# Performance work log

Hardware: AMD Instinct MI355X
Metric: run time of the kernel (lower is better)

The kernel has to match this reference:

```python
import jax, jax.numpy as jnp
import numpy as np

N, E, B, D = 8192, 32768, 64, 64   # nodes, edges, graphs, hidden dim
FN, FE, EH = 32, 16, 128           # node feat, edge feat, edge-MLP hidden
STEPS, S2S = 4, 5                  # message passes, set2set steps
EPS = 1e-5


def bn(x, g, b):
    # BatchNorm1d forward with batch statistics (training-mode math, biased var)
    m = x.mean(0)
    v = x.var(0)
    return (x - m) * jax.lax.rsqrt(v + EPS) * g + b


def setup_inputs() -> dict:
    key = jax.random.key(0)
    ks = iter(jax.random.split(key, 48))
    def nrm(shape, s=0.1):
        return jax.random.normal(next(ks), shape, jnp.float32) * s
    return {
        "x": jax.random.normal(next(ks), (N, FN), jnp.float32),
        "edge_attr": jax.random.normal(next(ks), (E, FE), jnp.float32),
        "edge_index": jax.random.randint(next(ks), (2, E), 0, N),
        "batch": jnp.sort(jax.random.randint(next(ks), (N,), 0, B)),
        "lin0_W": nrm((FN, D)), "lin0_b": nrm((D,)),
        "bn0_g": jnp.ones(D), "bn0_b": jnp.zeros(D),
        "e1_W": nrm((FE, EH)), "e1_b": nrm((EH,)),
        "ebn_g": jnp.ones(EH), "ebn_b": jnp.zeros(EH),
        "e2_W": nrm((EH, D * D), 0.02), "e2_b": nrm((D * D,), 0.02),
        "root_W": nrm((D, D)), "root_b": nrm((D,)),
        "gru_Wih": nrm((D, 3 * D)), "gru_Whh": nrm((D, 3 * D)),
        "gru_bih": nrm((3 * D,)), "gru_bhh": nrm((3 * D,)),
        "lstm_Wih": nrm((2 * D, 4 * D)), "lstm_Whh": nrm((D, 4 * D)),
        "lstm_bih": nrm((4 * D,)), "lstm_bhh": nrm((4 * D,)),
        "f1_W": nrm((2 * D, 256)), "f1_b": nrm((256,)), "f1_g": jnp.ones(256), "f1_bt": jnp.zeros(256),
        "f2_W": nrm((256, 128)), "f2_b": nrm((128,)), "f2_g": jnp.ones(128), "f2_bt": jnp.zeros(128),
        "f3_W": nrm((128, 32)), "f3_b": nrm((32,)), "f3_g": jnp.ones(32), "f3_bt": jnp.zeros(32),
        "fo_W": nrm((32, 1)), "fo_b": nrm((1,)),
    }


def _forward(x, edge_attr, edge_index, batch,
             lin0_W, lin0_b, bn0_g, bn0_b,
             e1_W, e1_b, ebn_g, ebn_b, e2_W, e2_b,
             root_W, root_b,
             gru_Wih, gru_Whh, gru_bih, gru_bhh,
             lstm_Wih, lstm_Whh, lstm_bih, lstm_bhh,
             f1_W, f1_b, f1_g, f1_bt,
             f2_W, f2_b, f2_g, f2_bt,
             f3_W, f3_b, f3_g, f3_bt,
             fo_W, fo_b):
    src, dst = edge_index[0], edge_index[1]

    x0 = jax.nn.relu(bn(x @ lin0_W + lin0_b, bn0_g, bn0_b))  # [N, D]

    # Edge NN: per-edge weight matrix [E, D, D] (edge_attr is constant across passes)
    eh = jax.nn.relu(bn(edge_attr @ e1_W + e1_b, ebn_g, ebn_b))
    We = (eh @ e2_W + e2_b).reshape(E, D, D)

    cnt = jnp.clip(jax.ops.segment_sum(jnp.ones((E,), x.dtype), dst, num_segments=N), 1.0)

    h = x0
    xo = x0
    for _ in range(STEPS):
        # NNConv (aggr='mean', root weight + bias) then ReLU
        msg = jnp.einsum('ei,eio->eo', xo[src], We)                     # [E, D]
        agg = jax.ops.segment_sum(msg, dst, num_segments=N) / cnt[:, None]
        m = jax.nn.relu(agg + xo @ root_W + root_b)
        # GRU cell (seq len 1): gates r, z, n
        gi = m @ gru_Wih + gru_bih
        gh = h @ gru_Whh + gru_bhh
        ir, iz, inn = jnp.split(gi, 3, -1)
        hr, hz, hn = jnp.split(gh, 3, -1)
        r = jax.nn.sigmoid(ir + hr)
        z = jax.nn.sigmoid(iz + hz)
        n = jnp.tanh(inn + r * hn)
        h = (1.0 - z) * n + z * h
        xo = h  # dropout is identity in eval mode

    # Set2Set pooling: LSTM + segment-softmax attention over ragged graphs
    qs = jnp.zeros((B, 2 * D), x.dtype)
    hl = jnp.zeros((B, D), x.dtype)
    cl = jnp.zeros((B, D), x.dtype)
    for _ in range(S2S):
        g = qs @ lstm_Wih + lstm_bih + hl @ lstm_Whh + lstm_bhh
        i_, f_, g_, o_ = jnp.split(g, 4, -1)
        cl = jax.nn.sigmoid(f_) * cl + jax.nn.sigmoid(i_) * jnp.tanh(g_)
        hl = jax.nn.sigmoid(o_) * jnp.tanh(cl)
        q = hl                                                           # [B, D]
        e = jnp.sum(xo * q[batch], -1)                                   # [N]
        emax = jax.lax.stop_gradient(jax.ops.segment_max(e, batch, num_segments=B))
        a = jnp.exp(e - emax[batch])
        a = a / (jax.ops.segment_sum(a, batch, num_segments=B)[batch] + 1e-16)
        rsum = jax.ops.segment_sum(a[:, None] * xo, batch, num_segments=B)
        qs = jnp.concatenate([q, rsum], -1)                              # [B, 2D]

    # FCNN head: Linear+BN+ReLU x3, then Linear -> 1
    y = jax.nn.relu(bn(qs @ f1_W + f1_b, f1_g, f1_bt))
    y = jax.nn.relu(bn(y @ f2_W + f2_b, f2_g, f2_bt))
    y = jax.nn.relu(bn(y @ f3_W + f3_b, f3_g, f3_bt))
    return (y @ fo_W + fo_b).reshape(-1)                                 # [B]


def reference(x, edge_attr, edge_index, batch,
              lin0_W, lin0_b, bn0_g, bn0_b,
              e1_W, e1_b, ebn_g, ebn_b, e2_W, e2_b,
              root_W, root_b,
              gru_Wih, gru_Whh, gru_bih, gru_bhh,
              lstm_Wih, lstm_Whh, lstm_bih, lstm_bhh,
              f1_W, f1_b, f1_g, f1_bt,
              f2_W, f2_b, f2_g, f2_bt,
              f3_W, f3_b, f3_g, f3_bt,
              fo_W, fo_b):
    return _forward(x, edge_attr, edge_index, batch,
                    lin0_W, lin0_b, bn0_g, bn0_b,
                    e1_W, e1_b, ebn_g, ebn_b, e2_W, e2_b,
                    root_W, root_b,
                    gru_Wih, gru_Whh, gru_bih, gru_bhh,
                    lstm_Wih, lstm_Whh, lstm_bih, lstm_bhh,
                    f1_W, f1_b, f1_g, f1_bt,
                    f2_W, f2_b, f2_g, f2_bt,
                    f3_W, f3_b, f3_g, f3_bt,
                    fo_W, fo_b)
```

## Files before the change

### kernel.cpp

```cpp
#include <hip/hip_runtime.h>
#include <hip/hip_bf16.h>


#define N_  8192
#define E_  32768
#define B_  64
#define D_  64
#define FN_ 32
#define FE_ 16
#define EH_ 128

typedef _Float16 half8 __attribute__((ext_vector_type(8)));
typedef float    f32x4 __attribute__((ext_vector_type(4)));

__device__ __forceinline__ float sigmf(float x) { return 1.f / (1.f + expf(-x)); }

#if __has_builtin(__builtin_amdgcn_global_load_lds)
#define HAVE_GLDS 1
__device__ __forceinline__ void gl2lds16(const void* g, void* l) {
  __builtin_amdgcn_global_load_lds(
      (const __attribute__((address_space(1))) void*)g,
      (__attribute__((address_space(3))) void*)l, 16, 0, 0);
}
#else
#define HAVE_GLDS 0
#endif


__global__ __launch_bounds__(256) void k_pre1(const float* __restrict__ x,
    const float* __restrict__ lin0W, const float* __restrict__ lin0b,
    const float* __restrict__ ea, const float* __restrict__ e1W, const float* __restrict__ e1b,
    const int* __restrict__ dstI, const int* __restrict__ batch,
    float* __restrict__ t0, float* __restrict__ t1,
    int* __restrict__ cnt_i, int* __restrict__ nodecnt) {
  const int bid = blockIdx.x, t = threadIdx.x;
  if (bid < 2048) {
    int gid = bid * 256 + t;
    int n = gid >> 6, d = gid & 63;
    const float* xr = x + (size_t)n * FN_;
    float a = lin0b[d];
    #pragma unroll
    for (int i = 0; i < FN_; ++i) a += xr[i] * lin0W[i * 64 + d];
    t0[gid] = a;
  } else if (bid < 18432) {
    int gid = (bid - 2048) * 256 + t;
    int n = gid >> 7, j = gid & 127;
    const float* er = ea + (size_t)n * FE_;
    float a = e1b[j];
    #pragma unroll
    for (int i = 0; i < FE_; ++i) a += er[i] * e1W[i * 128 + j];
    t1[gid] = a;
  } else if (bid < 18560) {
    atomicAdd(&cnt_i[dstI[(bid - 18432) * 256 + t]], 1);
  } else {
    atomicAdd(&nodecnt[batch[(bid - 18560) * 256 + t]], 1);
  }
}


__global__ __launch_bounds__(256) void k_stats(const float* __restrict__ t0,
    const float* __restrict__ t1, float* __restrict__ mean0, float* __restrict__ rstd0,
    float* __restrict__ meanE, float* __restrict__ rstdE) {
  const int bid = blockIdx.x;
  const float* in; int rows, cols, d; float* mo; float* ro;
  if (bid < 64) { in = t0; rows = N_; cols = 64; d = bid; mo = mean0; ro = rstd0; }
  else { in = t1; rows = E_; cols = 128; d = bid - 64; mo = meanE; ro = rstdE; }
  float s = 0.f, s2 = 0.f;
  for (int n = threadIdx.x; n < rows; n += 256) {
    float v = in[(size_t)n * cols + d];
    s += v; s2 += v * v;
  }
  #pragma unroll
  for (int off = 32; off; off >>= 1) { s += __shfl_xor(s, off); s2 += __shfl_xor(s2, off); }
  __shared__ float ls[4], ls2[4];
  int w = threadIdx.x >> 6;
  if ((threadIdx.x & 63) == 0) { ls[w] = s; ls2[w] = s2; }
  __syncthreads();
  if (threadIdx.x == 0) {
    float S = ls[0] + ls[1] + ls[2] + ls[3], S2 = ls2[0] + ls2[1] + ls2[2] + ls2[3];
    float mu = S / rows;
    float va = S2 / rows - mu * mu;
    mo[d] = mu;
    ro[d] = rsqrtf(va + 1e-5f);
  }
}


__global__ __launch_bounds__(256) void k_pre3(const float* __restrict__ t0,
    const float* __restrict__ mean0, const float* __restrict__ rstd0,
    const float* __restrict__ bn0g, const float* __restrict__ bn0b,
    float* __restrict__ x0, float* __restrict__ hb,
    const float* __restrict__ t1, const float* __restrict__ meanE,
    const float* __restrict__ rstdE, const float* __restrict__ ebng,
    const float* __restrict__ ebnb, _Float16* __restrict__ ehq,
    const float* __restrict__ e2W, half8* __restrict__ w2p8,
    const float* __restrict__ gWih, const float* __restrict__ gWhh,
    half8* __restrict__ pWih, half8* __restrict__ pWhh,
    const float* __restrict__ e2b, const float* __restrict__ rootW,
    half8* __restrict__ pE2R) {
  const int bid = blockIdx.x, t = threadIdx.x;
  if (bid < 2048) {
    int gid = bid * 256 + t;
    int d = gid & 63;
    float v = fmaxf(0.f, (t0[gid] - mean0[d]) * rstd0[d] * bn0g[d] + bn0b[d]);
    x0[gid] = v; hb[gid] = v;
  } else if (bid < 18432) {
    int gid = (bid - 2048) * 256 + t;
    int d = gid & 127;
    float v = fmaxf(0.f, (t1[gid] - meanE[d]) * rstdE[d] * ebng[d] + ebnb[d]);
    ehq[gid] = (_Float16)v;
  } else if (bid < 18688) {
    int tt = (bid - 18432) * 256 + t;
    int l = tt & 63, nf = (tt >> 6) & 3, kf = (tt >> 8) & 3, i = tt >> 10;
    half8 v;
    #pragma unroll
    for (int j = 0; j < 8; ++j) {
      int k = kf * 32 + ((l >> 4) << 3) + j;
      v[j] = (_Float16)e2W[(size_t)k * 4096 + i * 64 + (nf << 4) + (l & 15)];
    }
    w2p8[tt] = v;
  } else if (bid < 18700) {
    int tt2 = (bid - 18688) * 256 + t;
    int tab = (tt2 >= 1536);
    int rr = tab ? tt2 - 1536 : tt2;
    int lane = rr & 63, q = rr >> 6;
    int tile = q % 12, kf = q / 12;
    const float* W = tab ? gWhh : gWih;
    int col = tile * 16 + (lane & 15);
    half8 v;
    #pragma unroll
    for (int j = 0; j < 8; ++j) {
      int k = kf * 32 + ((lane >> 4) << 3) + j;
      v[j] = (_Float16)W[k * 192 + col];
    }
    (tab ? pWhh : pWih)[rr] = v;
  } else {
    int rr = (bid - 18700) * 256 + t;
    int lane = rr & 63, q = rr >> 6;
    int tile = q % 8, kf = q / 8;
    int col = tile * 16 + (lane & 15);
    half8 v;
    #pragma unroll
    for (int j = 0; j < 8; ++j) {
      int k = kf * 32 + ((lane >> 4) << 3) + j;
      v[j] = (_Float16)((col < 64) ? e2b[k * 64 + col] : rootW[k * 64 + (col - 64)]);
    }
    pE2R[rr] = v;
  }
}


__global__ __launch_bounds__(1024) void k_scans(const int* __restrict__ cnt,
    const int* __restrict__ nodecnt, int* __restrict__ row_start,
    int* __restrict__ cursor, float* __restrict__ cntf, int* __restrict__ gs) {
  __shared__ int sp[1024];
  int t = threadIdx.x;
  if (t == 0) {
    int a = 0;
    for (int b = 0; b < B_; ++b) { gs[b] = a; a += nodecnt[b]; }
    gs[B_] = a;
  }
  int v[8]; int s = 0;
  #pragma unroll
  for (int j = 0; j < 8; ++j) { v[j] = cnt[t * 8 + j]; s += v[j]; }
  sp[t] = s;
  __syncthreads();
  for (int off = 1; off < 1024; off <<= 1) {
    int a = (t >= off) ? sp[t - off] : 0;
    __syncthreads();
    sp[t] += a;
    __syncthreads();
  }
  int run = sp[t] - s;
  #pragma unroll
  for (int j = 0; j < 8; ++j) {
    row_start[t * 8 + j] = run;
    cursor[t * 8 + j] = run;
    cntf[t * 8 + j] = fmaxf(1.0f, (float)v[j]);
    run += v[j];
  }
  if (t == 1023) row_start[N_] = run;
}

__global__ __launch_bounds__(256) void k_fillnl(const int* __restrict__ dstI,
    int* __restrict__ cursor, int* __restrict__ csr,
    const float* __restrict__ x0, const float* __restrict__ e2b,
    const float* __restrict__ rootW, const float* __restrict__ rootb,
    float* __restrict__ P2, float* __restrict__ R) {
  const int bid = blockIdx.x, t = threadIdx.x;
  if (bid < 128) {
    int e = bid * 256 + t;
    int pos = atomicAdd(&cursor[dstI[e]], 1);
    csr[pos] = e;
  } else {
    int gid = (bid - 128) * 256 + t;
    int n = gid >> 6, d = gid & 63;
    const float* xr = x0 + (size_t)n * 64;
    float ap = 0.f, ar = rootb[d];
    #pragma unroll 8
    for (int i = 0; i < 64; ++i) {
      float xv = xr[i];
      ap += xv * e2b[i * 64 + d];
      ar += xv * rootW[i * 64 + d];
    }
    P2[gid] = ap; R[gid] = ar;
  }
}


__global__ __launch_bounds__(256) void k_msg(const _Float16* __restrict__ ehq,
    const half8* __restrict__ w2p8, const float* __restrict__ xo, const float* __restrict__ P2,
    const int* __restrict__ srcI, float* __restrict__ msg) {
  __shared__ half8 bbuf[2][1024];
  __shared__ float xs[64][65];
  __shared__ int ssrc[64];
  const int tid = threadIdx.x;
  const int lane = tid & 63;
  const int w = tid >> 6;
  const int be = blockIdx.x * 64;

  if (tid < 64) ssrc[tid] = srcI[be + tid];
#if HAVE_GLDS
  #pragma unroll
  for (int c = 0; c < 4; ++c) gl2lds16(w2p8 + c * 256 + tid, &bbuf[0][c * 256 + tid]);
#endif
  __syncthreads();
  for (int r = w; r < 64; r += 4) xs[r][lane] = xo[(size_t)ssrc[r] * 64 + lane];

  half8 A[4][4];
  #pragma unroll
  for (int rt = 0; rt < 4; ++rt) {
    const _Float16* ap = ehq + (size_t)(be + rt * 16 + (lane & 15)) * 128 + ((lane >> 4) << 3);
    #pragma unroll
    for (int kf = 0; kf < 4; ++kf) A[rt][kf] = *(const half8*)(ap + kf * 32);
  }
#if !HAVE_GLDS
  #pragma unroll
  for (int c = 0; c < 4; ++c) bbuf[0][c * 256 + tid] = w2p8[c * 256 + tid];
#endif

  f32x4 acc[4] = {{0.f,0.f,0.f,0.f},{0.f,0.f,0.f,0.f},{0.f,0.f,0.f,0.f},{0.f,0.f,0.f,0.f}};
  __syncthreads();

  for (int i = 0; i < 64; ++i) {
    const int inext = (i < 63) ? i + 1 : 63;
    const half8* gp = w2p8 + (size_t)inext * 1024;
#if HAVE_GLDS
    half8* nb = &bbuf[(i + 1) & 1][0];
    #pragma unroll
    for (int c = 0; c < 4; ++c) gl2lds16(gp + c * 256 + tid, nb + c * 256 + tid);
#else
    half8 p[4];
    #pragma unroll
    for (int c = 0; c < 4; ++c) p[c] = gp[c * 256 + tid];
#endif

    const half8* bb = bbuf[i & 1];
    half8 Bf[4];
    #pragma unroll
    for (int kf = 0; kf < 4; ++kf) Bf[kf] = bb[(kf * 4 + w) * 64 + lane];

    #pragma unroll
    for (int rt = 0; rt < 4; ++rt) {
      f32x4 C = {0.f, 0.f, 0.f, 0.f};
      #pragma unroll
      for (int kf = 0; kf < 4; ++kf)
        C = __builtin_amdgcn_mfma_f32_16x16x32_f16(A[rt][kf], Bf[kf], C, 0, 0, 0);
      const int rbase = rt * 16 + ((lane >> 4) << 2);
      #pragma unroll
      for (int r = 0; r < 4; ++r) acc[rt][r] += xs[rbase + r][i] * C[r];
    }
#if !HAVE_GLDS
    half8* nb = &bbuf[(i + 1) & 1][0];
    #pragma unroll
    for (int c = 0; c < 4; ++c) nb[c * 256 + tid] = p[c];
#endif
    __syncthreads();
  }

  const int col = (w << 4) + (lane & 15);
  #pragma unroll
  for (int rt = 0; rt < 4; ++rt) {
    const int rbase = rt * 16 + ((lane >> 4) << 2);
    #pragma unroll
    for (int r = 0; r < 4; ++r) {
      const int row = rbase + r;
      const int e = be + row;
      const int sn = ssrc[row];
      msg[(size_t)e * 64 + col] = acc[rt][r] + P2[(size_t)sn * 64 + col];
    }
  }
}


__global__ __launch_bounds__(256) void k_node(const float* __restrict__ msg,
    const int* __restrict__ csr, const int* __restrict__ row_start,
    const float* __restrict__ cntf,
    const half8* __restrict__ pWih, const half8* __restrict__ pWhh,
    const float* __restrict__ bih, const float* __restrict__ bhh,
    const half8* __restrict__ pE2R, const float* __restrict__ rootb,
    float* __restrict__ h, float* __restrict__ P2, float* __restrict__ R, int doPR) {
  __shared__ _Float16 sm16[16 * 72];
  __shared__ _Float16 sh16[16 * 72];
  __shared__ float sh32[16 * 64];
  __shared__ float sgi[16 * 208];
  __shared__ float sgh[16 * 208];
  const int t = threadIdx.x, lane = t & 63, w = t >> 6;
  const int n0 = blockIdx.x * 16;

  #pragma unroll
  for (int g = 0; g < 4; ++g) {
    int nl = g * 4 + w, n = n0 + nl;
    int e0 = row_start[n], e1 = row_start[n + 1];
    float acc = 0.f;
    for (int idx = e0; idx < e1; ++idx) acc += msg[(size_t)csr[idx] * 64 + lane];
    float mval = fmaxf(0.f, acc / cntf[n] + R[(size_t)n * 64 + lane]);
    float hval = h[(size_t)n * 64 + lane];
    sm16[nl * 72 + lane] = (_Float16)mval;
    sh16[nl * 72 + lane] = (_Float16)hval;
    sh32[nl * 64 + lane] = hval;
  }
  __syncthreads();

  {
    const _Float16* As = (w < 2) ? sm16 : sh16;
    const half8* pW = (w < 2) ? pWih : pWhh;
    float* sg_ = (w < 2) ? sgi : sgh;
    const int abase = (lane & 15) * 72 + ((lane >> 4) << 3);
    half8 A0 = *(const half8*)(As + abase);
    half8 A1 = *(const half8*)(As + abase + 32);
    const int tbase = (w & 1) * 6;
    #pragma unroll
    for (int tt = 0; tt < 6; ++tt) {
      int tile = tbase + tt;
      half8 B0 = pW[tile * 64 + lane];
      half8 B1 = pW[(12 + tile) * 64 + lane];
      f32x4 C = {0.f, 0.f, 0.f, 0.f};
      C = __builtin_amdgcn_mfma_f32_16x16x32_f16(A0, B0, C, 0, 0, 0);
      C = __builtin_amdgcn_mfma_f32_16x16x32_f16(A1, B1, C, 0, 0, 0);
      int col = tile * 16 + (lane & 15);
      int rb = (lane >> 4) << 2;
      #pragma unroll
      for (int r = 0; r < 4; ++r) sg_[(rb + r) * 208 + col] = C[r];
    }
  }
  __syncthreads();

  #pragma unroll
  for (int rep = 0; rep < 4; ++rep) {
    int idx = rep * 256 + t, j = idx >> 6, d = idx & 63;
    float rr = sigmf(sgi[j * 208 + d] + bih[d] + sgh[j * 208 + d] + bhh[d]);
    float zz = sigmf(sgi[j * 208 + 64 + d] + bih[64 + d] + sgh[j * 208 + 64 + d] + bhh[64 + d]);
    float nn = tanhf(sgi[j * 208 + 128 + d] + bih[128 + d]
                     + rr * (sgh[j * 208 + 128 + d] + bhh[128 + d]));
    float hv = (1.f - zz) * nn + zz * sh32[j * 64 + d];
    h[(size_t)(n0 + j) * 64 + d] = hv;
    sh16[j * 72 + d] = (_Float16)hv;
  }
  __syncthreads();

  if (doPR) {
    const int abase = (lane & 15) * 72 + ((lane >> 4) << 3);
    half8 A0 = *(const half8*)(sh16 + abase);
    half8 A1 = *(const half8*)(sh16 + abase + 32);
    #pragma unroll
    for (int tt = 0; tt < 2; ++tt) {
      int tile = w * 2 + tt;
      half8 B0 = pE2R[tile * 64 + lane];
      half8 B1 = pE2R[(8 + tile) * 64 + lane];
      f32x4 C = {0.f, 0.f, 0.f, 0.f};
      C = __builtin_amdgcn_mfma_f32_16x16x32_f16(A0, B0, C, 0, 0, 0);
      C = __builtin_amdgcn_mfma_f32_16x16x32_f16(A1, B1, C, 0, 0, 0);
      int c0 = tile * 16 + (lane & 15);
      int rb = (lane >> 4) << 2;
      #pragma unroll
      for (int r = 0; r < 4; ++r) {
        int n = n0 + rb + r;
        if (c0 < 64) P2[(size_t)n * 64 + c0] = C[r];
        else R[(size_t)n * 64 + (c0 - 64)] = C[r] + rootb[c0 - 64];
      }
    }
  }
}


#define SCAP 224

__global__ __launch_bounds__(256) void k_s2s(const float* __restrict__ xo,
    const int* __restrict__ gs,
    const float* __restrict__ Wih, const float* __restrict__ Whh,
    const float* __restrict__ bih, const float* __restrict__ bhh,
    float* __restrict__ qs_g) {
  __shared__ float sxo[SCAP * 65];
  __shared__ float sqs[128], shl[64], scl[64], sg[256];
  __shared__ float se[512];
  __shared__ float redm[4], ash[4], rsh[4][64];
  const int t = threadIdx.x;
  const int lane = t & 63, w = t >> 6;
  const int b = blockIdx.x;
  const int s0 = gs[b], cnt = gs[b + 1] - s0;
  const int cc = (cnt < SCAP) ? cnt : SCAP;

  for (int i = w; i < cc; i += 4) sxo[i * 65 + lane] = xo[(size_t)(s0 + i) * 64 + lane];
  if (t < 128) sqs[t] = 0.f;
  if (t < 64) { shl[t] = 0.f; scl[t] = 0.f; }
  __syncthreads();

  for (int it = 0; it < 5; ++it) {
    float a = bih[t] + bhh[t];
    #pragma unroll 8
    for (int k = 0; k < 128; ++k) a += sqs[k] * Wih[k * 256 + t];
    #pragma unroll 8
    for (int k = 0; k < 64; ++k)  a += shl[k] * Whh[k * 256 + t];
    sg[t] = a;
    __syncthreads();
    if (t < 64) {
      float i_ = sg[t], f_ = sg[64 + t], g_ = sg[128 + t], o_ = sg[192 + t];
      float cl = sigmf(f_) * scl[t] + sigmf(i_) * tanhf(g_);
      scl[t] = cl;
      shl[t] = sigmf(o_) * tanhf(cl);
    }
    __syncthreads();
    for (int i = t; i < cnt; i += 256) {
      float acc = 0.f;
      if (i < SCAP) {
        #pragma unroll 8
        for (int d = 0; d < 64; ++d) acc += sxo[i * 65 + d] * shl[d];
      } else {
        const float* xr = xo + (size_t)(s0 + i) * 64;
        #pragma unroll 8
        for (int d = 0; d < 64; ++d) acc += xr[d] * shl[d];
      }
      se[i] = acc;
    }
    __syncthreads();
    float mx = -INFINITY;
    for (int i = t; i < cnt; i += 256) mx = fmaxf(mx, se[i]);
    #pragma unroll
    for (int off = 32; off; off >>= 1) mx = fmaxf(mx, __shfl_xor(mx, off));
    if (lane == 0) redm[w] = mx;
    __syncthreads();
    const float gmax = fmaxf(fmaxf(redm[0], redm[1]), fmaxf(redm[2], redm[3]));
    float s = 0.f;
    for (int i = t; i < cnt; i += 256) {
      float aa = expf(se[i] - gmax);
      se[i] = aa;
      s += aa;
    }
    #pragma unroll
    for (int off = 32; off; off >>= 1) s += __shfl_xor(s, off);
    if (lane == 0) ash[w] = s;
    __syncthreads();
    const float gsum = ash[0] + ash[1] + ash[2] + ash[3];
    float racc = 0.f;
    for (int i = w; i < cnt; i += 4) {
      float aa = se[i];
      racc += (i < SCAP) ? aa * sxo[i * 65 + lane]
                         : aa * xo[(size_t)(s0 + i) * 64 + lane];
    }
    rsh[w][lane] = racc;
    __syncthreads();
    if (t < 64) {
      float rt_ = rsh[0][t] + rsh[1][t] + rsh[2][t] + rsh[3][t];
      sqs[t] = shl[t];
      sqs[64 + t] = rt_ / (gsum + 1e-16f);
    }
    __syncthreads();
  }
  if (t < 128) qs_g[b * 128 + t] = sqs[t];
}


__global__ __launch_bounds__(256) void k_fc(const float* __restrict__ in,
    const float* __restrict__ W, const float* __restrict__ bias,
    const float* __restrict__ g, const float* __restrict__ bt,
    float* __restrict__ out, int K, int NC) {
  __shared__ float sin_[64 * 257];
  const int t = threadIdx.x, lane = t & 63, w = t >> 6;
  const int c = blockIdx.x * 4 + w;
  const int Kp = K + 1;
  for (int idx = t; idx < 64 * K; idx += 256) sin_[(idx / K) * Kp + (idx % K)] = in[idx];
  __syncthreads();
  float acc = 0.f;
  const float* wc = W + c;
  #pragma unroll 8
  for (int k = 0; k < K; ++k) acc += sin_[lane * Kp + k] * wc[(size_t)k * NC];
  acc += bias[c];
  float s = acc, s2 = acc * acc;
  #pragma unroll
  for (int off = 32; off; off >>= 1) { s += __shfl_xor(s, off); s2 += __shfl_xor(s2, off); }
  float mu = s * (1.f / 64.f);
  float rs = rsqrtf(s2 * (1.f / 64.f) - mu * mu + 1e-5f);
  out[(size_t)lane * NC + c] = fmaxf(0.f, (acc - mu) * rs * g[c] + bt[c]);
}

__global__ __launch_bounds__(256) void k_f3fo(const float* __restrict__ y2,
    const float* __restrict__ f3W, const float* __restrict__ f3b,
    const float* __restrict__ f3g, const float* __restrict__ f3bt,
    const float* __restrict__ foW, const float* __restrict__ fob,
    float* __restrict__ out) {
  __shared__ float sin_[64 * 129];
  __shared__ float sy3[64 * 33];
  const int t = threadIdx.x, lane = t & 63, w = t >> 6;
  for (int idx = t; idx < 64 * 128; idx += 256) sin_[(idx >> 7) * 129 + (idx & 127)] = y2[idx];
  __syncthreads();
  #pragma unroll
  for (int cg = 0; cg < 8; ++cg) {
    int c = w * 8 + cg;
    float acc = 0.f;
    #pragma unroll 8
    for (int k = 0; k < 128; ++k) acc += sin_[lane * 129 + k] * f3W[k * 32 + c];
    acc += f3b[c];
    float s = acc, s2 = acc * acc;
    #pragma unroll
    for (int off = 32; off; off >>= 1) { s += __shfl_xor(s, off); s2 += __shfl_xor(s2, off); }
    float mu = s * (1.f / 64.f);
    float rs = rsqrtf(s2 * (1.f / 64.f) - mu * mu + 1e-5f);
    sy3[lane * 33 + c] = fmaxf(0.f, (acc - mu) * rs * f3g[c] + f3bt[c]);
  }
  __syncthreads();
  if (t < 64) {
    float v = fob[0];
    #pragma unroll
    for (int k = 0; k < 32; ++k) v += sy3[t * 33 + k] * foW[k];
    out[t] = v;
  }
}


extern "C" void kernel_launch(void* const* d_in, const int* in_sizes, int n_in,
                              void* d_out, int out_size, void* d_ws, size_t ws_size,
                              hipStream_t stream) {
  (void)in_sizes; (void)n_in; (void)out_size; (void)ws_size;
  const float* x      = (const float*)d_in[0];
  const float* eattr  = (const float*)d_in[1];
  const int*   ei     = (const int*)d_in[2];
  const int*   batch  = (const int*)d_in[3];
  const float* lin0_W = (const float*)d_in[4];
  const float* lin0_b = (const float*)d_in[5];
  const float* bn0_g  = (const float*)d_in[6];
  const float* bn0_b  = (const float*)d_in[7];
  const float* e1_W   = (const float*)d_in[8];
  const float* e1_b   = (const float*)d_in[9];
  const float* ebn_g  = (const float*)d_in[10];
  const float* ebn_b  = (const float*)d_in[11];
  const float* e2_W   = (const float*)d_in[12];
  const float* e2_b   = (const float*)d_in[13];
  const float* root_W = (const float*)d_in[14];
  const float* root_b = (const float*)d_in[15];
  const float* gWih   = (const float*)d_in[16];
  const float* gWhh   = (const float*)d_in[17];
  const float* gbih   = (const float*)d_in[18];
  const float* gbhh   = (const float*)d_in[19];
  const float* lWih   = (const float*)d_in[20];
  const float* lWhh   = (const float*)d_in[21];
  const float* lbih   = (const float*)d_in[22];
  const float* lbhh   = (const float*)d_in[23];
  const float* f1_W   = (const float*)d_in[24];
  const float* f1_b   = (const float*)d_in[25];
  const float* f1_g   = (const float*)d_in[26];
  const float* f1_bt  = (const float*)d_in[27];
  const float* f2_W   = (const float*)d_in[28];
  const float* f2_b   = (const float*)d_in[29];
  const float* f2_g   = (const float*)d_in[30];
  const float* f2_bt  = (const float*)d_in[31];
  const float* f3_W   = (const float*)d_in[32];
  const float* f3_b   = (const float*)d_in[33];
  const float* f3_g   = (const float*)d_in[34];
  const float* f3_bt  = (const float*)d_in[35];
  const float* fo_W   = (const float*)d_in[36];
  const float* fo_b   = (const float*)d_in[37];
  const int* srcI = ei;
  const int* dstI = ei + E_;

  char* base = (char*)d_ws;
  size_t off = 0;
  auto alloc = [&](size_t bytes) -> void* {
    off = (off + 255) & ~(size_t)255;
    void* p = base + off;
    off += bytes;
    return p;
  };
  float* t0    = (float*)alloc((size_t)N_ * 64 * 4);
  float* t1    = (float*)alloc((size_t)E_ * 128 * 4);
  float* x0    = (float*)alloc((size_t)N_ * 64 * 4);
  float* hb    = (float*)alloc((size_t)N_ * 64 * 4);
  _Float16* ehq = (_Float16*)alloc((size_t)E_ * 128 * 2);
  half8* w2p8  = (half8*)alloc((size_t)65536 * 16);
  half8* pWih  = (half8*)alloc((size_t)1536 * 16);
  half8* pWhh  = (half8*)alloc((size_t)1536 * 16);
  half8* pE2R  = (half8*)alloc((size_t)1024 * 16);
  float* P2    = (float*)alloc((size_t)N_ * 64 * 4);
  float* R     = (float*)alloc((size_t)N_ * 64 * 4);
  float* msg   = (float*)alloc((size_t)E_ * 64 * 4);
  int* cnt_i   = (int*)alloc((size_t)N_ * 4);
  int* cursor  = (int*)alloc((size_t)N_ * 4);
  int* row_start = (int*)alloc((size_t)(N_ + 1) * 4);
  int* csr     = (int*)alloc((size_t)E_ * 4);
  float* cntf  = (float*)alloc((size_t)N_ * 4);
  int* nodecnt = (int*)alloc(64 * 4);
  int* gs      = (int*)alloc(65 * 4);
  float* mean0 = (float*)alloc(64 * 4);
  float* rstd0 = (float*)alloc(64 * 4);
  float* meanE = (float*)alloc(128 * 4);
  float* rstdE = (float*)alloc(128 * 4);
  float* qs    = (float*)alloc((size_t)B_ * 128 * 4);
  float* y1    = (float*)alloc((size_t)B_ * 256 * 4);
  float* y2    = (float*)alloc((size_t)B_ * 128 * 4);

  hipMemsetAsync(cnt_i, 0, (size_t)N_ * 4, stream);
  hipMemsetAsync(nodecnt, 0, 64 * 4, stream);

  k_pre1<<<18592, 256, 0, stream>>>(x, lin0_W, lin0_b, eattr, e1_W, e1_b,
                                    dstI, batch, t0, t1, cnt_i, nodecnt);
  k_stats<<<192, 256, 0, stream>>>(t0, t1, mean0, rstd0, meanE, rstdE);
  k_pre3<<<18704, 256, 0, stream>>>(t0, mean0, rstd0, bn0_g, bn0_b, x0, hb,
                                    t1, meanE, rstdE, ebn_g, ebn_b, ehq, e2_W, w2p8,
                                    gWih, gWhh, pWih, pWhh, e2_b, root_W, pE2R);
  k_scans<<<1, 1024, 0, stream>>>(cnt_i, nodecnt, row_start, cursor, cntf, gs);
  k_fillnl<<<2176, 256, 0, stream>>>(dstI, cursor, csr, x0, e2_b, root_W, root_b, P2, R);

  for (int s = 0; s < 4; ++s) {
    k_msg<<<E_ / 64, 256, 0, stream>>>(ehq, w2p8, (s == 0) ? x0 : hb, P2, srcI, msg);
    k_node<<<N_ / 16, 256, 0, stream>>>(msg, csr, row_start, cntf,
                                        pWih, pWhh, gbih, gbhh, pE2R, root_b,
                                        hb, P2, R, (s < 3) ? 1 : 0);
  }

  k_s2s<<<B_, 256, 0, stream>>>(hb, gs, lWih, lWhh, lbih, lbhh, qs);
  k_fc<<<64, 256, 0, stream>>>(qs, f1_W, f1_b, f1_g, f1_bt, y1, 128, 256);
  k_fc<<<32, 256, 0, stream>>>(y1, f2_W, f2_b, f2_g, f2_bt, y2, 256, 128);
  k_f3fo<<<1, 256, 0, stream>>>(y2, f3_W, f3_b, f3_g, f3_bt, fo_W, fo_b, (float*)d_out);
}
```

Measured before the change: 668.3 us.

## Vectorize preprocessing kernels and split BN statistics into coalesced two-stage reduction

The lin0 and edge-MLP first-layer kernels now compute 4 or 8 output columns per thread with float4 loads and stores, and the BN-apply kernel does the same, writing half8 for the edge features. This cuts the block count about sevenfold. The column-strided BN statistics kernel becomes a coalesced per-block partial-sum pass (k_statsP). Its final reduction is folded into the existing single-block scan kernel, which now runs before k_pre3. The aim is to remove the uncoalesced 192-block stats pass and reduce per-thread overhead in the preprocessing stages, at the cost of an extra partial buffer and more serial work in the one-block scan kernel.

```diff
diff --git a/kernel.cpp b/kernel.cpp
--- a/kernel.cpp
+++ b/kernel.cpp
@@ -34,55 +34,141 @@
     float* __restrict__ t0, float* __restrict__ t1,
     int* __restrict__ cnt_i, int* __restrict__ nodecnt) {
   const int bid = blockIdx.x, t = threadIdx.x;
-  if (bid < 2048) {
+  if (bid < 512) {
     int gid = bid * 256 + t;
-    int n = gid >> 6, d = gid & 63;
+    int n = gid >> 4, d4 = (gid & 15) * 4;
     const float* xr = x + (size_t)n * FN_;
-    float a = lin0b[d];
-    #pragma unroll
-    for (int i = 0; i < FN_; ++i) a += xr[i] * lin0W[i * 64 + d];
-    t0[gid] = a;
-  } else if (bid < 18432) {
-    int gid = (bid - 2048) * 256 + t;
-    int n = gid >> 7, j = gid & 127;
+    f32x4 a = *(const f32x4*)&lin0b[d4];
+    #pragma unroll
+    for (int i = 0; i < FN_; ++i)
+      a += xr[i] * *(const f32x4*)&lin0W[i * 64 + d4];
+    *(f32x4*)&t0[(size_t)n * 64 + d4] = a;
+  } else if (bid < 2560) {
+    int gid = (bid - 512) * 256 + t;
+    int n = gid >> 4, j8 = (gid & 15) * 8;
     const float* er = ea + (size_t)n * FE_;
-    float a = e1b[j];
-    #pragma unroll
-    for (int i = 0; i < FE_; ++i) a += er[i] * e1W[i * 128 + j];
-    t1[gid] = a;
-  } else if (bid < 18560) {
-    atomicAdd(&cnt_i[dstI[(bid - 18432) * 256 + t]], 1);
+    f32x4 a0 = *(const f32x4*)&e1b[j8];
+    f32x4 a1 = *(const f32x4*)&e1b[j8 + 4];
+    #pragma unroll
+    for (int i = 0; i < FE_; ++i) {
+      float ev = er[i];
+      a0 += ev * *(const f32x4*)&e1W[i * 128 + j8];
+      a1 += ev * *(const f32x4*)&e1W[i * 128 + j8 + 4];
+    }
+    *(f32x4*)&t1[(size_t)n * 128 + j8] = a0;
+    *(f32x4*)&t1[(size_t)n * 128 + j8 + 4] = a1;
+  } else if (bid < 2688) {
+    atomicAdd(&cnt_i[dstI[(bid - 2560) * 256 + t]], 1);
   } else {
-    atomicAdd(&nodecnt[batch[(bid - 18560) * 256 + t]], 1);
-  }
-}
-
-
-__global__ __launch_bounds__(256) void k_stats(const float* __restrict__ t0,
-    const float* __restrict__ t1, float* __restrict__ mean0, float* __restrict__ rstd0,
+    atomicAdd(&nodecnt[batch[(bid - 2688) * 256 + t]], 1);
+  }
+}
+
+
+__global__ __launch_bounds__(256) void k_statsP(const float* __restrict__ t0,
+    const float* __restrict__ t1, float* __restrict__ pT, float* __restrict__ pE) {
+  __shared__ float red[256][8];
+  const int bid = blockIdx.x, t = threadIdx.x;
+  if (bid < 16) {
+    const f32x4* v = (const f32x4*)t0;
+    f32x4 s = {0.f,0.f,0.f,0.f}, s2 = {0.f,0.f,0.f,0.f};
+    #pragma unroll 8
+    for (int it = 0; it < 32; ++it) {
+      f32x4 xv = v[bid * 8192 + it * 256 + t];
+      s += xv; s2 += xv * xv;
+    }
+    #pragma unroll
+    for (int j = 0; j < 4; ++j) { red[t][j] = s[j]; red[t][4 + j] = s2[j]; }
+    __syncthreads();
+    if (t < 64) {
+      int g = t >> 2, comp = t & 3;
+      float a = 0.f, b = 0.f;
+      #pragma unroll
+      for (int k = 0; k < 16; ++k) { a += red[g + k * 16][comp]; b += red[g + k * 16][4 + comp]; }
+      pT[bid * 128 + t] = a;
+      pT[bid * 128 + 64 + t] = b;
+    }
+  } else {
+    int eb = bid - 16;
+    const f32x4* v = (const f32x4*)t1;
+    f32x4 s = {0.f,0.f,0.f,0.f}, s2 = {0.f,0.f,0.f,0.f};
+    #pragma unroll
+    for (int it = 0; it < 16; ++it) {
+      f32x4 xv = v[eb * 4096 + it * 256 + t];
+      s += xv; s2 += xv * xv;
+    }
+    #pragma unroll
+    for (int j = 0; j < 4; ++j) { red[t][j] = s[j]; red[t][4 + j] = s2[j]; }
+    __syncthreads();
+    if (t < 128) {
+      int g = t >> 2, comp = t & 3;
+      float a = 0.f, b = 0.f;
+      #pragma unroll
+      for (int k = 0; k < 8; ++k) { a += red[g + k * 32][comp]; b += red[g + k * 32][4 + comp]; }
+      pE[eb * 256 + t] = a;
+      pE[eb * 256 + 128 + t] = b;
+    }
+  }
+}
+
+
+__global__ __launch_bounds__(1024) void k_scans(const int* __restrict__ cnt,
+    const int* __restrict__ nodecnt, int* __restrict__ row_start,
+    int* __restrict__ cursor, float* __restrict__ cntf, int* __restrict__ gs,
+    const float* __restrict__ pT, const float* __restrict__ pE,
+    float* __restrict__ mean0, float* __restrict__ rstd0,
     float* __restrict__ meanE, float* __restrict__ rstdE) {
-  const int bid = blockIdx.x;
-  const float* in; int rows, cols, d; float* mo; float* ro;
-  if (bid < 64) { in = t0; rows = N_; cols = 64; d = bid; mo = mean0; ro = rstd0; }
-  else { in = t1; rows = E_; cols = 128; d = bid - 64; mo = meanE; ro = rstdE; }
-  float s = 0.f, s2 = 0.f;
-  for (int n = threadIdx.x; n < rows; n += 256) {
-    float v = in[(size_t)n * cols + d];
-    s += v; s2 += v * v;
-  }
-  #pragma unroll
-  for (int off = 32; off; off >>= 1) { s += __shfl_xor(s, off); s2 += __shfl_xor(s2, off); }
-  __shared__ float ls[4], ls2[4];
-  int w = threadIdx.x >> 6;
-  if ((threadIdx.x & 63) == 0) { ls[w] = s; ls2[w] = s2; }
-  __syncthreads();
-  if (threadIdx.x == 0) {
-    float S = ls[0] + ls[1] + ls[2] + ls[3], S2 = ls2[0] + ls2[1] + ls2[2] + ls2[3];
-    float mu = S / rows;
-    float va = S2 / rows - mu * mu;
-    mo[d] = mu;
-    ro[d] = rsqrtf(va + 1e-5f);
-  }
+  __shared__ int sp[1024];
+  int t = threadIdx.x;
+  {
+    int c = t >> 3, k0 = t & 7;
+    float s = 0.f, q = 0.f;
+    for (int b = k0; b < 256; b += 8) { s += pE[b * 256 + c]; q += pE[b * 256 + 128 + c]; }
+    s += __shfl_xor(s, 1); s += __shfl_xor(s, 2); s += __shfl_xor(s, 4);
+    q += __shfl_xor(q, 1); q += __shfl_xor(q, 2); q += __shfl_xor(q, 4);
+    if (k0 == 0) {
+      float mu = s / (float)E_;
+      meanE[c] = mu;
+      rstdE[c] = rsqrtf(q / (float)E_ - mu * mu + 1e-5f);
+    }
+    if (t < 512) {
+      int c2 = t >> 3, k2 = t & 7;
+      float s3 = pT[k2 * 128 + c2] + pT[(k2 + 8) * 128 + c2];
+      float q3 = pT[k2 * 128 + 64 + c2] + pT[(k2 + 8) * 128 + 64 + c2];
+      s3 += __shfl_xor(s3, 1); s3 += __shfl_xor(s3, 2); s3 += __shfl_xor(s3, 4);
+      q3 += __shfl_xor(q3, 1); q3 += __shfl_xor(q3, 2); q3 += __shfl_xor(q3, 4);
+      if (k2 == 0) {
+        float mu = s3 / (float)N_;
+        mean0[c2] = mu;
+        rstd0[c2] = rsqrtf(q3 / (float)N_ - mu * mu + 1e-5f);
+      }
+    }
+  }
+  if (t == 0) {
+    int a = 0;
+    for (int b = 0; b < B_; ++b) { gs[b] = a; a += nodecnt[b]; }
+    gs[B_] = a;
+  }
+  int v[8]; int s = 0;
+  #pragma unroll
+  for (int j = 0; j < 8; ++j) { v[j] = cnt[t * 8 + j]; s += v[j]; }
+  sp[t] = s;
+  __syncthreads();
+  for (int off = 1; off < 1024; off <<= 1) {
+    int a = (t >= off) ? sp[t - off] : 0;
+    __syncthreads();
+    sp[t] += a;
+    __syncthreads();
+  }
+  int run = sp[t] - s;
+  #pragma unroll
+  for (int j = 0; j < 8; ++j) {
+    row_start[t * 8 + j] = run;
+    cursor[t * 8 + j] = run;
+    cntf[t * 8 + j] = fmaxf(1.0f, (float)v[j]);
+    run += v[j];
+  }
+  if (t == 1023) row_start[N_] = run;
 }
 
 
@@ -99,18 +185,37 @@
     const float* __restrict__ e2b, const float* __restrict__ rootW,
     half8* __restrict__ pE2R) {
   const int bid = blockIdx.x, t = threadIdx.x;
-  if (bid < 2048) {
+  if (bid < 512) {
     int gid = bid * 256 + t;
-    int d = gid & 63;
-    float v = fmaxf(0.f, (t0[gid] - mean0[d]) * rstd0[d] * bn0g[d] + bn0b[d]);
-    x0[gid] = v; hb[gid] = v;
-  } else if (bid < 18432) {
-    int gid = (bid - 2048) * 256 + t;
-    int d = gid & 127;
-    float v = fmaxf(0.f, (t1[gid] - meanE[d]) * rstdE[d] * ebng[d] + ebnb[d]);
-    ehq[gid] = (_Float16)v;
-  } else if (bid < 18688) {
-    int tt = (bid - 18432) * 256 + t;
+    int n = gid >> 4, d4 = (gid & 15) * 4;
+    f32x4 v  = *(const f32x4*)&t0[(size_t)n * 64 + d4];
+    f32x4 mu = *(const f32x4*)&mean0[d4];
+    f32x4 rs = *(const f32x4*)&rstd0[d4];
+    f32x4 gg = *(const f32x4*)&bn0g[d4];
+    f32x4 bb = *(const f32x4*)&bn0b[d4];
+    f32x4 r = (v - mu) * rs * gg + bb;
+    #pragma unroll
+    for (int j = 0; j < 4; ++j) r[j] = fmaxf(0.f, r[j]);
+    *(f32x4*)&x0[(size_t)n * 64 + d4] = r;
+    *(f32x4*)&hb[(size_t)n * 64 + d4] = r;
+  } else if (bid < 2560) {
+    int gid = (bid - 512) * 256 + t;
+    int n = gid >> 4, j8 = (gid & 15) * 8;
+    half8 o;
+    #pragma unroll
+    for (int hc = 0; hc < 2; ++hc) {
+      f32x4 v  = *(const f32x4*)&t1[(size_t)n * 128 + j8 + hc * 4];
+      f32x4 mu = *(const f32x4*)&meanE[j8 + hc * 4];
+      f32x4 rs = *(const f32x4*)&rstdE[j8 + hc * 4];
+      f32x4 gg = *(const f32x4*)&ebng[j8 + hc * 4];
+      f32x4 bb = *(const f32x4*)&ebnb[j8 + hc * 4];
+      f32x4 r = (v - mu) * rs * gg + bb;
+      #pragma unroll
+      for (int j = 0; j < 4; ++j) o[hc * 4 + j] = (_Float16)fmaxf(0.f, r[j]);
+    }
+    *(half8*)&ehq[(size_t)n * 128 + j8] = o;
+  } else if (bid < 2816) {
+    int tt = (bid - 2560) * 256 + t;
     int l = tt & 63, nf = (tt >> 6) & 3, kf = (tt >> 8) & 3, i = tt >> 10;
     half8 v;
     #pragma unroll
@@ -119,8 +224,8 @@
       v[j] = (_Float16)e2W[(size_t)k * 4096 + i * 64 + (nf << 4) + (l & 15)];
     }
     w2p8[tt] = v;
-  } else if (bid < 18700) {
-    int tt2 = (bid - 18688) * 256 + t;
+  } else if (bid < 2828) {
+    int tt2 = (bid - 2816) * 256 + t;
     int tab = (tt2 >= 1536);
     int rr = tab ? tt2 - 1536 : tt2;
     int lane = rr & 63, q = rr >> 6;
@@ -135,7 +240,7 @@
     }
     (tab ? pWhh : pWih)[rr] = v;
   } else {
-    int rr = (bid - 18700) * 256 + t;
+    int rr = (bid - 2828) * 256 + t;
     int lane = rr & 63, q = rr >> 6;
     int tile = q % 8, kf = q / 8;
     int col = tile * 16 + (lane & 15);
@@ -149,38 +254,6 @@
   }
 }
 
-
-__global__ __launch_bounds__(1024) void k_scans(const int* __restrict__ cnt,
-    const int* __restrict__ nodecnt, int* __restrict__ row_start,
-    int* __restrict__ cursor, float* __restrict__ cntf, int* __restrict__ gs) {
-  __shared__ int sp[1024];
-  int t = threadIdx.x;
-  if (t == 0) {
-    int a = 0;
-    for (int b = 0; b < B_; ++b) { gs[b] = a; a += nodecnt[b]; }
-    gs[B_] = a;
-  }
-  int v[8]; int s = 0;
-  #pragma unroll
-  for (int j = 0; j < 8; ++j) { v[j] = cnt[t * 8 + j]; s += v[j]; }
-  sp[t] = s;
-  __syncthreads();
-  for (int off = 1; off < 1024; off <<= 1) {
-    int a = (t >= off) ? sp[t - off] : 0;
-    __syncthreads();
-    sp[t] += a;
-    __syncthreads();
-  }
-  int run = sp[t] - s;
-  #pragma unroll
-  for (int j = 0; j < 8; ++j) {
-    row_start[t * 8 + j] = run;
-    cursor[t * 8 + j] = run;
-    cntf[t * 8 + j] = fmaxf(1.0f, (float)v[j]);
-    run += v[j];
-  }
-  if (t == 1023) row_start[N_] = run;
-}
 
 __global__ __launch_bounds__(256) void k_fillnl(const int* __restrict__ dstI,
     int* __restrict__ cursor, int* __restrict__ csr,
@@ -604,6 +677,8 @@
   float* rstd0 = (float*)alloc(64 * 4);
   float* meanE = (float*)alloc(128 * 4);
   float* rstdE = (float*)alloc(128 * 4);
+  float* pT    = (float*)alloc((size_t)16 * 128 * 4);
+  float* pE    = (float*)alloc((size_t)256 * 256 * 4);
   float* qs    = (float*)alloc((size_t)B_ * 128 * 4);
   float* y1    = (float*)alloc((size_t)B_ * 256 * 4);
   float* y2    = (float*)alloc((size_t)B_ * 128 * 4);
@@ -611,13 +686,14 @@
   hipMemsetAsync(cnt_i, 0, (size_t)N_ * 4, stream);
   hipMemsetAsync(nodecnt, 0, 64 * 4, stream);
 
-  k_pre1<<<18592, 256, 0, stream>>>(x, lin0_W, lin0_b, eattr, e1_W, e1_b,
-                                    dstI, batch, t0, t1, cnt_i, nodecnt);
-  k_stats<<<192, 256, 0, stream>>>(t0, t1, mean0, rstd0, meanE, rstdE);
-  k_pre3<<<18704, 256, 0, stream>>>(t0, mean0, rstd0, bn0_g, bn0_b, x0, hb,
-                                    t1, meanE, rstdE, ebn_g, ebn_b, ehq, e2_W, w2p8,
-                                    gWih, gWhh, pWih, pWhh, e2_b, root_W, pE2R);
-  k_scans<<<1, 1024, 0, stream>>>(cnt_i, nodecnt, row_start, cursor, cntf, gs);
+  k_pre1<<<2720, 256, 0, stream>>>(x, lin0_W, lin0_b, eattr, e1_W, e1_b,
+                                   dstI, batch, t0, t1, cnt_i, nodecnt);
+  k_statsP<<<272, 256, 0, stream>>>(t0, t1, pT, pE);
+  k_scans<<<1, 1024, 0, stream>>>(cnt_i, nodecnt, row_start, cursor, cntf, gs,
+                                  pT, pE, mean0, rstd0, meanE, rstdE);
+  k_pre3<<<2832, 256, 0, stream>>>(t0, mean0, rstd0, bn0_g, bn0_b, x0, hb,
+                                   t1, meanE, rstdE, ebn_g, ebn_b, ehq, e2_W, w2p8,
+                                   gWih, gWhh, pWih, pWhh, e2_b, root_W, pE2R);
   k_fillnl<<<2176, 256, 0, stream>>>(dstI, cursor, csr, x0, e2_b, root_W, root_b, P2, R);
 
   for (int s = 0; s < 4; ++s) {
```

New measurement: 622.0 us. -6.9%, faster.
